# Performance work log

Hardware: AMD Instinct MI355X
Metric: run time of the kernel (lower is better)

## Reference

```python
import jax, jax.numpy as jnp
import numpy as np

B, W, H, L, D = 4, 32, 32, 32, 256
K, S, V = 24, 16384, 8  # heads, selected positions per head, logits per head
N = B * W * H * L


def setup_inputs() -> dict:
    key = jax.random.key(0)
    k1, k2, k3, k4, k5 = jax.random.split(key, 5)
    block_type_grid = jax.random.randint(k1, (B, W, H, L), 0, 800, dtype=jnp.int32)
    features = jax.random.normal(k2, (B, W, H, L, D), dtype=jnp.float32)
    mask_idx = jax.random.randint(k3, (K, S), 0, N, dtype=jnp.int32)
    head_weights = jax.random.normal(k4, (K, D, V), dtype=jnp.float32) * (1.0 / np.sqrt(D))
    head_bias = jax.random.normal(k5, (K, V), dtype=jnp.float32) * 0.01
    return {
        "block_type_grid": block_type_grid,
        "features": features,
        "mask_idx": mask_idx,
        "head_weights": head_weights,
        "head_bias": head_bias,
    }


def reference(block_type_grid, features, mask_idx, head_weights, head_bias):
    # Flatten spatial grid: (B,W,H,L,D) -> (N,D)
    feats_flat = features.reshape(-1, D)
    # Grouped boolean-mask gather (as fixed-size index gather): (K,S,D)
    gathered = feats_flat[mask_idx]
    # Per-head small Linear: logits[k,s,v] = gathered[k,s,:] @ W[k,:,v] + b[k,v]
    logits = jnp.einsum('ksd,kdv->ksv', gathered, head_weights) + head_bias[:, None, :]
    return logits
```

## Files before the change

kernel.cpp:

```cpp
#include <hip/hip_runtime.h>


#define KH 24
#define SS 16384
#define VV 8
#define DD 256

template <int CTRL>
__device__ __forceinline__ float dpp_mov(float x) {
    int xi = __builtin_bit_cast(int, x);
    int r = __builtin_amdgcn_update_dpp(xi, xi, CTRL, 0xF, 0xF, false);
    return __builtin_bit_cast(float, r);
}

__device__ __forceinline__ float reduce8(const float acc[8], int lane) {
    const bool b0 = lane & 1;
    const bool b1 = lane & 2;
    const bool b2 = lane & 4;

    float a4[4];
#pragma unroll
    for (int j = 0; j < 4; ++j) {
        const float keep = b0 ? acc[2 * j + 1] : acc[2 * j];
        const float send = b0 ? acc[2 * j] : acc[2 * j + 1];
        a4[j] = keep + dpp_mov<0xB1>(send);
    }
    float a2[2];
#pragma unroll
    for (int m = 0; m < 2; ++m) {
        const float keep = b1 ? a4[2 * m + 1] : a4[2 * m];
        const float send = b1 ? a4[2 * m] : a4[2 * m + 1];
        a2[m] = keep + dpp_mov<0x4E>(send);
    }
    {
        const float keep = b2 ? a2[1] : a2[0];
        const float send = b2 ? a2[0] : a2[1];
        float a1 = keep + __shfl_xor(send, 4, 64);
        a1 += dpp_mov<0x128>(a1);
        a1 += __shfl_xor(a1, 16, 64);
        a1 += __shfl_xor(a1, 32, 64);
        return a1;
    }
}

__global__ __launch_bounds__(256) void attr_decoder_kernel(
    const float* __restrict__ feats,
    const int*   __restrict__ mask_idx,
    const float* __restrict__ head_w,
    const float* __restrict__ head_b,
    float*       __restrict__ out)
{
    const int lane  = threadIdx.x & 63;
    const int wv    = threadIdx.x >> 6;
    const int k     = blockIdx.x >> 7;
    const int chunk = blockIdx.x & 127;

    const float* Wk = head_w + (size_t)k * (DD * VV);
    float w[4][8];
#pragma unroll
    for (int t = 0; t < 4; ++t) {
        const float4 a = *(const float4*)(Wk + (lane * 4 + t) * VV);
        const float4 b = *(const float4*)(Wk + (lane * 4 + t) * VV + 4);
        w[t][0] = a.x; w[t][1] = a.y; w[t][2] = a.z; w[t][3] = a.w;
        w[t][4] = b.x; w[t][5] = b.y; w[t][6] = b.z; w[t][7] = b.w;
    }
    const float bias = head_b[k * VV + (lane & 7)];

    const float4* feats4 = (const float4*)feats;
    const int s_base = chunk * 128 + wv * 32;
    const int* mi = mask_idx + k * SS + s_base;
    float* outp = out + ((size_t)k * SS + s_base) * VV;

    const int g = (lane >> 3) & 3;

    for (int i = 0; i < 32; i += 4) {
        const int4 rows = *(const int4*)(mi + i);
        const float4 f0 = feats4[(size_t)rows.x * 64 + lane];
        const float4 f1 = feats4[(size_t)rows.y * 64 + lane];
        const float4 f2 = feats4[(size_t)rows.z * 64 + lane];
        const float4 f3 = feats4[(size_t)rows.w * 64 + lane];

        float r[4];
        const float4 f[4] = {f0, f1, f2, f3};
#pragma unroll
        for (int u = 0; u < 4; ++u) {
            float acc[8];
#pragma unroll
            for (int v = 0; v < 8; ++v) {
                acc[v] = f[u].x * w[0][v];
                acc[v] = fmaf(f[u].y, w[1][v], acc[v]);
                acc[v] = fmaf(f[u].z, w[2][v], acc[v]);
                acc[v] = fmaf(f[u].w, w[3][v], acc[v]);
            }
            r[u] = reduce8(acc, lane);
        }

        const float r01 = (g & 1) ? r[1] : r[0];
        const float r23 = (g & 1) ? r[3] : r[2];
        const float val = ((g & 2) ? r23 : r01) + bias;
        if (lane < 32) outp[i * VV + lane] = val;
    }
}

extern "C" void kernel_launch(void* const* d_in, const int* in_sizes, int n_in,
                              void* d_out, int out_size, void* d_ws, size_t ws_size,
                              hipStream_t stream) {
    const float* feats    = (const float*)d_in[1];
    const int*   mask_idx = (const int*)  d_in[2];
    const float* head_w   = (const float*)d_in[3];
    const float* head_b   = (const float*)d_in[4];
    float* out = (float*)d_out;

    dim3 grid(KH * 128);
    dim3 block(256);
    attr_decoder_kernel<<<grid, block, 0, stream>>>(feats, mask_idx, head_w, head_b, out);
}
```

Measured before the change: 230.5 us.

## Compute dense per-row logits with bf16 MFMA, then gather selected rows

```diff
diff --git a/kernel.cpp b/kernel.cpp
--- a/kernel.cpp
+++ b/kernel.cpp
@@ -5,6 +5,106 @@
 #define SS 16384
 #define VV 8
 #define DD 256
+#define NG 192
+#define NROWS 131072
+
+typedef short bf16x8 __attribute__((ext_vector_type(8)));
+typedef float f32x4  __attribute__((ext_vector_type(4)));
+typedef int   i32x4  __attribute__((ext_vector_type(4)));
+
+__device__ __forceinline__ unsigned short f32_bf16_rne(float f) {
+    unsigned u = __builtin_bit_cast(unsigned, f);
+    u = (u + 0x7FFFu + ((u >> 16) & 1u)) >> 16;
+    return (unsigned short)u;
+}
+
+__device__ __forceinline__ unsigned pack_bf16x2(float lo, float hi) {
+    unsigned ulo = __builtin_bit_cast(unsigned, lo) + 0x8000u;
+    unsigned uhi = __builtin_bit_cast(unsigned, hi) + 0x8000u;
+    return __builtin_amdgcn_perm(uhi, ulo, 0x07060302);
+}
+
+__global__ __launch_bounds__(256, 3) void dense_logits_kernel(
+    const float* __restrict__ feats,
+    const float* __restrict__ head_w,
+    const float* __restrict__ head_b,
+    unsigned short* __restrict__ logits)
+{
+    const int lane = threadIdx.x & 63;
+    const int wv   = threadIdx.x >> 6;
+    const int n    = lane & 15;
+    const int q    = lane >> 4;
+
+    bf16x8 Bf[3][8];
+    float  bias_v[3];
+#pragma unroll
+    for (int tile = 0; tile < 3; ++tile) {
+        const int n_g = wv * 48 + tile * 16 + n;
+        const float* Wh = head_w + (size_t)(n_g >> 3) * (DD * VV) + (n_g & 7);
+#pragma unroll
+        for (int t = 0; t < 8; ++t)
+#pragma unroll
+            for (int j = 0; j < 8; ++j)
+                Bf[tile][t][j] = (short)f32_bf16_rne(Wh[(t * 32 + q * 8 + j) * VV]);
+        bias_v[tile] = head_b[(n_g >> 3) * VV + (n_g & 7)];
+    }
+
+    const int rbase = blockIdx.x * 256;
+#pragma unroll 1
+    for (int mt = 0; mt < 16; ++mt) {
+        const int mbase = rbase + mt * 16;
+        const float* p = feats + (size_t)(mbase + n) * DD + q * 8;
+
+        f32x4 acc[3];
+#pragma unroll
+        for (int tile = 0; tile < 3; ++tile) {
+            const float b = bias_v[tile];
+            acc[tile][0] = b; acc[tile][1] = b; acc[tile][2] = b; acc[tile][3] = b;
+        }
+#pragma unroll
+        for (int t = 0; t < 8; ++t) {
+            const float4 a0 = *(const float4*)(p + t * 32);
+            const float4 a1 = *(const float4*)(p + t * 32 + 4);
+            i32x4 ai;
+            ai[0] = (int)pack_bf16x2(a0.x, a0.y);
+            ai[1] = (int)pack_bf16x2(a0.z, a0.w);
+            ai[2] = (int)pack_bf16x2(a1.x, a1.y);
+            ai[3] = (int)pack_bf16x2(a1.z, a1.w);
+            const bf16x8 a = __builtin_bit_cast(bf16x8, ai);
+            acc[0] = __builtin_amdgcn_mfma_f32_16x16x32_bf16(a, Bf[0][t], acc[0], 0, 0, 0);
+            acc[1] = __builtin_amdgcn_mfma_f32_16x16x32_bf16(a, Bf[1][t], acc[1], 0, 0, 0);
+            acc[2] = __builtin_amdgcn_mfma_f32_16x16x32_bf16(a, Bf[2][t], acc[2], 0, 0, 0);
+        }
+#pragma unroll
+        for (int tile = 0; tile < 3; ++tile) {
+            const int n_g = wv * 48 + tile * 16 + n;
+            unsigned short* op = logits + (size_t)(mbase + q * 4) * NG + n_g;
+#pragma unroll
+            for (int i = 0; i < 4; ++i)
+                op[(size_t)i * NG] = f32_bf16_rne(acc[tile][i]);
+        }
+    }
+}
+
+__global__ __launch_bounds__(256) void gather_logits_kernel(
+    const unsigned short* __restrict__ logits,
+    const int* __restrict__ mask_idx,
+    float* __restrict__ out)
+{
+    const int tid  = blockIdx.x * 256 + threadIdx.x;
+    const int gsel = tid >> 1;
+    const int half = tid & 1;
+    const int k    = gsel >> 14;
+    const int idx  = mask_idx[gsel];
+    const unsigned short* lp = logits + (size_t)idx * NG + k * VV + half * 4;
+    const ushort4 u = *(const ushort4*)lp;
+    float4 r;
+    r.x = __builtin_bit_cast(float, (unsigned)u.x << 16);
+    r.y = __builtin_bit_cast(float, (unsigned)u.y << 16);
+    r.z = __builtin_bit_cast(float, (unsigned)u.z << 16);
+    r.w = __builtin_bit_cast(float, (unsigned)u.w << 16);
+    *(float4*)(out + (size_t)gsel * VV + half * 4) = r;
+}
 
 template <int CTRL>
 __device__ __forceinline__ float dpp_mov(float x) {
@@ -17,7 +117,6 @@
     const bool b0 = lane & 1;
     const bool b1 = lane & 2;
     const bool b2 = lane & 4;
-
     float a4[4];
 #pragma unroll
     for (int j = 0; j < 4; ++j) {
@@ -32,29 +131,24 @@
         const float send = b1 ? a4[2 * m] : a4[2 * m + 1];
         a2[m] = keep + dpp_mov<0x4E>(send);
     }
-    {
-        const float keep = b2 ? a2[1] : a2[0];
-        const float send = b2 ? a2[0] : a2[1];
-        float a1 = keep + __shfl_xor(send, 4, 64);
-        a1 += dpp_mov<0x128>(a1);
-        a1 += __shfl_xor(a1, 16, 64);
-        a1 += __shfl_xor(a1, 32, 64);
-        return a1;
-    }
-}
-
-__global__ __launch_bounds__(256) void attr_decoder_kernel(
-    const float* __restrict__ feats,
-    const int*   __restrict__ mask_idx,
-    const float* __restrict__ head_w,
-    const float* __restrict__ head_b,
-    float*       __restrict__ out)
+    const float keep = b2 ? a2[1] : a2[0];
+    const float send = b2 ? a2[0] : a2[1];
+    float a1 = keep + __shfl_xor(send, 4, 64);
+    a1 += dpp_mov<0x128>(a1);
+    a1 += __shfl_xor(a1, 16, 64);
+    a1 += __shfl_xor(a1, 32, 64);
+    return a1;
+}
+
+__global__ __launch_bounds__(256) void attr_decoder_fallback(
+    const float* __restrict__ feats, const int* __restrict__ mask_idx,
+    const float* __restrict__ head_w, const float* __restrict__ head_b,
+    float* __restrict__ out)
 {
     const int lane  = threadIdx.x & 63;
-    const int wv    = threadIdx.x >> 6;
+    const int wvv   = threadIdx.x >> 6;
     const int k     = blockIdx.x >> 7;
     const int chunk = blockIdx.x & 127;
-
     const float* Wk = head_w + (size_t)k * (DD * VV);
     float w[4][8];
 #pragma unroll
@@ -65,21 +159,17 @@
         w[t][4] = b.x; w[t][5] = b.y; w[t][6] = b.z; w[t][7] = b.w;
     }
     const float bias = head_b[k * VV + (lane & 7)];
-
     const float4* feats4 = (const float4*)feats;
-    const int s_base = chunk * 128 + wv * 32;
+    const int s_base = chunk * 128 + wvv * 32;
     const int* mi = mask_idx + k * SS + s_base;
     float* outp = out + ((size_t)k * SS + s_base) * VV;
-
     const int g = (lane >> 3) & 3;
-
     for (int i = 0; i < 32; i += 4) {
         const int4 rows = *(const int4*)(mi + i);
         const float4 f0 = feats4[(size_t)rows.x * 64 + lane];
         const float4 f1 = feats4[(size_t)rows.y * 64 + lane];
         const float4 f2 = feats4[(size_t)rows.z * 64 + lane];
         const float4 f3 = feats4[(size_t)rows.w * 64 + lane];
-
         float r[4];
         const float4 f[4] = {f0, f1, f2, f3};
 #pragma unroll
@@ -94,7 +184,6 @@
             }
             r[u] = reduce8(acc, lane);
         }
-
         const float r01 = (g & 1) ? r[1] : r[0];
         const float r23 = (g & 1) ? r[3] : r[2];
         const float val = ((g & 2) ? r23 : r01) + bias;
@@ -111,7 +200,15 @@
     const float* head_b   = (const float*)d_in[4];
     float* out = (float*)d_out;
 
-    dim3 grid(KH * 128);
-    dim3 block(256);
-    attr_decoder_kernel<<<grid, block, 0, stream>>>(feats, mask_idx, head_w, head_b, out);
-}
+    const size_t need = (size_t)NROWS * NG * sizeof(unsigned short);
+    if (ws_size >= need) {
+        unsigned short* logits = (unsigned short*)d_ws;
+        dense_logits_kernel<<<dim3(NROWS / 256), dim3(256), 0, stream>>>(
+            feats, head_w, head_b, logits);
+        gather_logits_kernel<<<dim3(KH * SS * 2 / 256), dim3(256), 0, stream>>>(
+            logits, mask_idx, out);
+    } else {
+        attr_decoder_fallback<<<dim3(KH * 128), dim3(256), 0, stream>>>(
+            feats, mask_idx, head_w, head_b, out);
+    }
+}
```

Result: slower. 283.8 us (+23.1%).
